# Kernel tuning notes

Measured on AMD Instinct MI355X. Metric: run time of the kernel, lower is better.

## Reference

```python
import jax, jax.numpy as jnp
import numpy as np

N_USER = 100000
N_ITEM = 100000
SUPP = 10000
B = 1024
L = 50
S = 256
H = 4
E = 64
HID = 64


def setup_inputs() -> dict:
    key = jax.random.key(0)
    ks = jax.random.split(key, 32)
    f32 = jnp.float32
    inp = {}
    # forward int args
    inp["x"] = jax.random.randint(ks[0], (B, 2), 0, N_USER)
    inp["src_his"] = jax.random.randint(ks[1], (B, L), 0, N_ITEM)
    inp["src_hl"] = jax.random.randint(ks[2], (B,), 0, L)
    inp["tgt_his"] = jax.random.randint(ks[3], (B, L), 0, N_ITEM)
    inp["tgt_hl"] = jax.random.randint(ks[4], (B,), 0, L)
    # precomputed neighbor sampling: [2 get_user_emb calls, H heads, B, S]
    inp["sample_idx"] = jax.random.randint(ks[5], (2, H, B, S), 0, SUPP)
    inp["supp_users"] = jax.random.randint(ks[6], (SUPP,), 0, N_USER)
    # embedding tables (xavier-ish small scale)
    inp["src_user_emb"] = jax.random.normal(ks[7], (N_USER, E), f32) * 0.1
    inp["src_item_emb"] = jax.random.normal(ks[8], (N_ITEM, E), f32) * 0.1
    inp["tgt_user_emb"] = jax.random.normal(ks[9], (N_USER, E), f32) * 0.1
    inp["tgt_item_emb"] = jax.random.normal(ks[10], (N_ITEM, E), f32) * 0.1
    # attention / aggregation weights, stored [in, out]
    s = 1.0 / np.sqrt(E)
    inp["W_att_w"] = jax.random.normal(ks[11], (E, E), f32) * s
    inp["W_att_b"] = jnp.full((E,), 0.1, f32)
    inp["W_agg_w"] = jax.random.normal(ks[12], (E, E), f32) * s
    # per-head GAT projections, batched over heads
    inp["Wq"] = jax.random.normal(ks[13], (H, E, E), f32) * s
    inp["Wk"] = jax.random.normal(ks[14], (H, E, E), f32) * s
    inp["Wv"] = jax.random.normal(ks[15], (H, E, E), f32) * s
    inp["W_out"] = jax.random.normal(ks[16], (H * E, E), f32) * (1.0 / np.sqrt(H * E))
    # scoring MLP
    inp["l1_w"] = jax.random.normal(ks[17], (2 * E, HID), f32) * (1.0 / np.sqrt(2 * E))
    inp["l1_b"] = jnp.full((HID,), 0.1, f32)
    inp["l2_w"] = jax.random.normal(ks[18], (HID, E), f32) * (1.0 / np.sqrt(HID))
    inp["l2_b"] = jnp.full((E,), 0.1, f32)
    inp["l3_w"] = jax.random.normal(ks[19], (E, 1), f32) * s
    inp["l3_b"] = jnp.full((1,), 0.1, f32)
    return inp


def reference(x, src_his, src_hl, tgt_his, tgt_hl, sample_idx, supp_users,
              src_user_emb, src_item_emb, tgt_user_emb, tgt_item_emb,
              W_att_w, W_att_b, W_agg_w, Wq, Wk, Wv, W_out,
              l1_w, l1_b, l2_w, l2_b, l3_w, l3_b):
    user_id = x[:, 0]
    item_id = x[:, 1]

    def user_fea_encode(his, hl, user_table):
        # NOTE: original always gathers from src_model.item_embedding (even for tgt)
        Lh = his.shape[1]
        valid = jnp.arange(Lh)[None, :] < hl[:, None]          # [B,L]
        hist = src_item_emb[his] * valid[..., None]             # [B,L,E], padded rows zeroed
        u = user_table[user_id]                                 # [B,E]
        keyt = jnp.tanh(hist @ W_att_w + W_att_b)               # [B,L,E]
        pad = hist.sum(-1) == 0                                 # [B,L]
        att = jnp.einsum('ble,be->bl', keyt, u)
        # faithful masked_softmax: masked scores set to 0 BEFORE exp (exp(0)=1 still contributes)
        att = jnp.where(pad, 0.0, att)
        e = jnp.exp(att)
        att = e / (jnp.sum(e, axis=1, keepdims=True) + 1e-12)
        out = jnp.einsum('bl,ble->be', att, hist)
        return out @ W_agg_w                                    # W_agg has no bias

    def get_user_emb(fea, idx):
        # idx: [H,B,S] indices into supp_users; all heads batched in one einsum chain
        neigh = tgt_user_emb[supp_users[idx]]                   # [H,B,S,E]
        q = jnp.einsum('be,heo->hbo', fea, Wq)                  # [H,B,O]
        k = jnp.einsum('hbse,heo->hbso', neigh, Wk)             # [H,B,S,O]
        attn = jax.nn.softmax(jnp.einsum('hbo,hbso->hbs', q, k), axis=-1)
        ctx = jnp.einsum('hbs,hbso->hbo', attn, k)              # weighted sum over neighbors
        g = jnp.einsum('hbo,hop->hbp', ctx, Wv)                 # [H,B,O]
        g = jnp.transpose(g, (1, 0, 2)).reshape(fea.shape[0], -1)  # concat heads -> [B,H*O]
        return g @ W_out

    user_src_fea = user_fea_encode(src_his, src_hl, src_user_emb)
    user_emb = get_user_emb(user_src_fea, sample_idx[0])
    item_emb = tgt_item_emb[item_id]
    user_tgt_fea = user_fea_encode(tgt_his, tgt_hl, tgt_user_emb)
    hybrid_tgt_emb = get_user_emb(user_tgt_fea, sample_idx[1])

    x_t = jnp.concatenate([hybrid_tgt_emb, item_emb], axis=1)
    x1_t = jnp.tanh(x_t @ l1_w + l1_b)
    x2_t = jnp.tanh(x1_t @ l2_w + l2_b)
    x3_t = (x2_t @ l3_w + l3_b).reshape(-1)

    output = jnp.sum(user_emb * item_emb, axis=1)
    out_emb_s = user_emb * item_emb
    # (output, output_t, out_emb_s, out_emb_t); train=False branch (sim/domain heads are None)
    return (output, x3_t, out_emb_s, x2_t)
```

## Files before the change

### kernel.cpp

```cpp
#include <hip/hip_runtime.h>

constexpr int B    = 1024;
constexpr int L    = 50;
constexpr int S    = 256;
constexpr int H    = 4;
constexpr int E    = 64;
constexpr int HID  = 64;
constexpr int SUPP = 10000;

__device__ __forceinline__ float lanebc(float v, int l) {
    return __int_as_float(__builtin_amdgcn_readlane(__float_as_int(v), l));
}

__device__ __forceinline__ float bcdot64(float v, const float* w) {
    float a0 = 0.0f, a1 = 0.0f;
#pragma unroll
    for (int i = 0; i < E; i += 2) {
        a0 += lanebc(v, i)     * w[i];
        a1 += lanebc(v, i + 1) * w[i + 1];
    }
    return a0 + a1;
}

__global__ __launch_bounds__(256) void pre_kernel(
    const int* __restrict__ x,
    const int* __restrict__ src_his,
    const int* __restrict__ src_hl,
    const int* __restrict__ tgt_his,
    const int* __restrict__ tgt_hl,
    const float* __restrict__ item_emb,
    const float* __restrict__ src_user_emb,
    const float* __restrict__ tgt_user_emb,
    const int* __restrict__ supp_users,
    const float* __restrict__ W_att_w,
    const float* __restrict__ W_att_b,
    const float* __restrict__ W_agg_w,
    const float* __restrict__ Wq,
    const float* __restrict__ Wk,
    float* __restrict__ qout,
    float* __restrict__ K_supp)
{
    const int tid  = threadIdx.x;
    const int lane = tid & 63;
    const int wave = tid >> 6;

    if (blockIdx.y == 2) {
        const int h = wave;
        float wcol[E];
#pragma unroll
        for (int i = 0; i < E; i++) wcol[i] = Wk[h * E * E + i * E + lane];

        const int base = blockIdx.x * 4;
#pragma unroll
        for (int m = 0; m < 3; m++) {
            const int j0 = base + m * 4096;
            if (j0 >= SUPP) break;
            const int u0 = supp_users[j0];
            const int u1 = supp_users[j0 + 1];
            const int u2 = supp_users[j0 + 2];
            const int u3 = supp_users[j0 + 3];
            const float e0 = tgt_user_emb[(size_t)u0 * E + lane];
            const float e1 = tgt_user_emb[(size_t)u1 * E + lane];
            const float e2 = tgt_user_emb[(size_t)u2 * E + lane];
            const float e3 = tgt_user_emb[(size_t)u3 * E + lane];
            float a0 = 0.0f, a1 = 0.0f, a2 = 0.0f, a3 = 0.0f;
#pragma unroll
            for (int i = 0; i < E; i++) {
                a0 += lanebc(e0, i) * wcol[i];
                a1 += lanebc(e1, i) * wcol[i];
                a2 += lanebc(e2, i) * wcol[i];
                a3 += lanebc(e3, i) * wcol[i];
            }
            float* dst = K_supp + ((size_t)h * SUPP + j0) * E + lane;
            dst[0]     = a0;
            dst[E]     = a1;
            dst[2 * E] = a2;
            dst[3 * E] = a3;
        }
        return;
    }

    __shared__ float sHist[L * E];
    __shared__ float sAtt[L];
    __shared__ float sPart[4][E];
    __shared__ float sOut[E];

    const int b    = blockIdx.x;
    const int call = blockIdx.y;

    const int* his = call ? tgt_his : src_his;
    const int* hl  = call ? tgt_hl  : src_hl;
    const float* user_table = call ? tgt_user_emb : src_user_emb;

    float wcol[E];
#pragma unroll
    for (int i = 0; i < E; i++) wcol[i] = W_att_w[i * E + lane];

    const int uid    = x[2 * b];
    const float uv   = user_table[(size_t)uid * E + lane];
    const float bias = W_att_b[lane];
    const int hlen   = hl[b];

#pragma unroll
    for (int i = 0; i < 13; i++) {
        const int l = wave + 4 * i;
        if (l < L) {
            const int it = his[b * L + l];
            sHist[l * E + lane] = (l < hlen) ? item_emb[(size_t)it * E + lane] : 0.0f;
        }
    }
    __syncthreads();

#pragma unroll
    for (int g = 0; g < 3; g++) {
        const int l0 = wave + 16 * g;
        const int l1 = l0 + 4, l2 = l0 + 8, l3 = l0 + 12;
        const float h0 = sHist[l0 * E + lane];
        const float h1 = sHist[l1 * E + lane];
        const float h2 = sHist[l2 * E + lane];
        const float h3 = sHist[l3 * E + lane];
        float a0 = bias, a1 = bias, a2 = bias, a3 = bias;
#pragma unroll
        for (int i = 0; i < E; i++) {
            a0 += lanebc(h0, i) * wcol[i];
            a1 += lanebc(h1, i) * wcol[i];
            a2 += lanebc(h2, i) * wcol[i];
            a3 += lanebc(h3, i) * wcol[i];
        }
        float p0 = tanhf(a0) * uv, p1 = tanhf(a1) * uv;
        float p2 = tanhf(a2) * uv, p3 = tanhf(a3) * uv;
        float s0 = h0, s1 = h1, s2 = h2, s3 = h3;
#pragma unroll
        for (int off = 32; off; off >>= 1) {
            p0 += __shfl_xor(p0, off); s0 += __shfl_xor(s0, off);
            p1 += __shfl_xor(p1, off); s1 += __shfl_xor(s1, off);
            p2 += __shfl_xor(p2, off); s2 += __shfl_xor(s2, off);
            p3 += __shfl_xor(p3, off); s3 += __shfl_xor(s3, off);
        }
        if (lane == 0) {
            sAtt[l0] = (s0 == 0.0f) ? 0.0f : p0;
            sAtt[l1] = (s1 == 0.0f) ? 0.0f : p1;
            sAtt[l2] = (s2 == 0.0f) ? 0.0f : p2;
            sAtt[l3] = (s3 == 0.0f) ? 0.0f : p3;
        }
    }
    {
        const int l = wave + 48;
        if (l < L) {
            const float hv = sHist[l * E + lane];
            const float a = bias + bcdot64(hv, wcol);
            float part = tanhf(a) * uv;
            float hsum = hv;
#pragma unroll
            for (int off = 32; off; off >>= 1) {
                part += __shfl_xor(part, off);
                hsum += __shfl_xor(hsum, off);
            }
            if (lane == 0) sAtt[l] = (hsum == 0.0f) ? 0.0f : part;
        }
    }
    __syncthreads();

    if (wave == 0) {
        float v = (lane < L) ? expf(sAtt[lane]) : 0.0f;
        float s = v;
#pragma unroll
        for (int off = 32; off; off >>= 1) s += __shfl_xor(s, off);
        const float denom = s + 1e-12f;
        if (lane < L) sAtt[lane] = v / denom;
    }
    __syncthreads();

    {
        float c0 = 0.0f, c1 = 0.0f;
        for (int l = wave; l < L; l += 8) c0 += sAtt[l] * sHist[l * E + lane];
        for (int l = wave + 4; l < L; l += 8) c1 += sAtt[l] * sHist[l * E + lane];
        sPart[wave][lane] = c0 + c1;
    }
    __syncthreads();
    if (tid < E) sOut[tid] = sPart[0][tid] + sPart[1][tid] + sPart[2][tid] + sPart[3][tid];
    __syncthreads();

    {
        float g0 = 0.0f, g1 = 0.0f;
#pragma unroll
        for (int k = 0; k < 16; k += 2) {
            const int i = wave * 16 + k;
            g0 += sOut[i]     * W_agg_w[i * E + lane];
            g1 += sOut[i + 1] * W_agg_w[(i + 1) * E + lane];
        }
        sPart[wave][lane] = g0 + g1;
    }
    __syncthreads();

    const float fval = sPart[0][lane] + sPart[1][lane] + sPart[2][lane] + sPart[3][lane];
    const float* Wqh = Wq + wave * E * E;
    float q0 = 0.0f, q1 = 0.0f;
#pragma unroll
    for (int i = 0; i < E; i += 2) {
        q0 += lanebc(fval, i)     * Wqh[i * E + lane];
        q1 += lanebc(fval, i + 1) * Wqh[(i + 1) * E + lane];
    }
    qout[(((call * H) + wave) * B + b) * E + lane] = q0 + q1;
}

__global__ __launch_bounds__(256) void attn_kernel(
    const int* __restrict__ sample_idx,
    const float* __restrict__ K_supp,
    const float* __restrict__ qarr,
    const float* __restrict__ Wv,
    float* __restrict__ gout)
{
    __shared__ float sRed[8];
    __shared__ float sCtx[4][E];
    __shared__ float sC[E];
    __shared__ float sG[4][E];

    const int bid  = blockIdx.x;
    const int h    = bid & 3;
    const int call = (bid >> 2) & 1;
    const int b    = bid >> 3;
    const int tid  = threadIdx.x;
    const int lane = tid & 63;
    const int wave = tid >> 6;
    const int u    = lane & 15;
    const int rsub = lane >> 4;
    const int s0   = wave * 64;

    const int* idx = sample_idx + (((call * H) + h) * B + b) * S;
    const float* Kh = K_supp + (size_t)h * SUPP * E;
    const float4 qu = *(const float4*)(qarr + ((size_t)(((call * H) + h) * B + b)) * E + 4 * u);

    float4 kreg[16];
    float mylogit = 0.0f;
#pragma unroll
    for (int i = 0; i < 16; i++) {
        const int j = idx[s0 + 4 * i + rsub];
        kreg[i] = *(const float4*)(Kh + (size_t)j * E + 4 * u);
        float part = kreg[i].x * qu.x + kreg[i].y * qu.y
                   + kreg[i].z * qu.z + kreg[i].w * qu.w;
#pragma unroll
        for (int off = 1; off < 16; off <<= 1) part += __shfl_xor(part, off);
        mylogit = (u == i) ? part : mylogit;
    }

    float m = mylogit;
#pragma unroll
    for (int off = 32; off; off >>= 1) m = fmaxf(m, __shfl_xor(m, off));
    if (lane == 0) sRed[wave] = m;
    __syncthreads();
    const float mx = fmaxf(fmaxf(sRed[0], sRed[1]), fmaxf(sRed[2], sRed[3]));
    const float ex = expf(mylogit - mx);
    float sm = ex;
#pragma unroll
    for (int off = 32; off; off >>= 1) sm += __shfl_xor(sm, off);
    if (lane == 0) sRed[4 + wave] = sm;
    __syncthreads();
    const float denom = sRed[4] + sRed[5] + sRed[6] + sRed[7];
    const float pval = ex / denom;

    float4 cacc = make_float4(0.0f, 0.0f, 0.0f, 0.0f);
#pragma unroll
    for (int i = 0; i < 16; i++) {
        const float p = __shfl(pval, (lane & 48) + i);
        cacc.x += p * kreg[i].x;
        cacc.y += p * kreg[i].y;
        cacc.z += p * kreg[i].z;
        cacc.w += p * kreg[i].w;
    }
#pragma unroll
    for (int off = 16; off <= 32; off <<= 1) {
        cacc.x += __shfl_xor(cacc.x, off);
        cacc.y += __shfl_xor(cacc.y, off);
        cacc.z += __shfl_xor(cacc.z, off);
        cacc.w += __shfl_xor(cacc.w, off);
    }
    if (lane < 16) *(float4*)(&sCtx[wave][u * 4]) = cacc;
    __syncthreads();
    if (wave == 0) {
        sC[lane] = sCtx[0][lane] + sCtx[1][lane] + sCtx[2][lane] + sCtx[3][lane];
    }
    __syncthreads();

    const float* Wvh = Wv + h * E * E;
    float g0 = 0.0f, g1 = 0.0f;
#pragma unroll
    for (int k = 0; k < 16; k += 2) {
        const int c = wave * 16 + k;
        g0 += sC[c]     * Wvh[c * E + lane];
        g1 += sC[c + 1] * Wvh[(c + 1) * E + lane];
    }
    sG[wave][lane] = g0 + g1;
    __syncthreads();
    if (wave == 0) {
        gout[((size_t)(call * B) + b) * (H * E) + h * E + lane] =
            sG[0][lane] + sG[1][lane] + sG[2][lane] + sG[3][lane];
    }
}

__global__ __launch_bounds__(256) void final_kernel(
    const int* __restrict__ x,
    const float* __restrict__ tgt_item_emb,
    const float* __restrict__ gsrc,
    const float* __restrict__ gtgt,
    const float* __restrict__ W_out,
    const float* __restrict__ l1_w,
    const float* __restrict__ l1_b,
    const float* __restrict__ l2_w,
    const float* __restrict__ l2_b,
    const float* __restrict__ l3_w,
    const float* __restrict__ l3_b,
    float* __restrict__ out)
{
    __shared__ float sPart[4][E];
    __shared__ float sHyb[E];
    __shared__ float sItem[E];
    __shared__ float sX1[HID];

    const int b    = blockIdx.x;
    const int tid  = threadIdx.x;
    const int lane = tid & 63;
    const int wave = tid >> 6;

    if (tid < E) {
        const int item = x[2 * b + 1];
        sItem[tid] = tgt_item_emb[(size_t)item * E + tid];
    }

    const float* grow = (wave < 2) ? (gsrc + (size_t)b * (H * E))
                                   : (gtgt + (size_t)b * (H * E));
    const int i0 = (wave & 1) * 128;
    float a0 = 0.0f, a1 = 0.0f, a2 = 0.0f, a3 = 0.0f;
    for (int i = i0; i < i0 + 128; i += 4) {
        a0 += grow[i]     * W_out[i * E + lane];
        a1 += grow[i + 1] * W_out[(i + 1) * E + lane];
        a2 += grow[i + 2] * W_out[(i + 2) * E + lane];
        a3 += grow[i + 3] * W_out[(i + 3) * E + lane];
    }
    sPart[wave][lane] = (a0 + a1) + (a2 + a3);
    __syncthreads();

    if (wave == 0) {
        const float ue = sPart[0][lane] + sPart[1][lane];
        const float prod = ue * sItem[lane];
        out[2 * B + b * E + lane] = prod;
        float s = prod;
#pragma unroll
        for (int off = 32; off; off >>= 1) s += __shfl_xor(s, off);
        if (lane == 0) out[b] = s;
    }
    if (wave == 1) {
        sHyb[lane] = sPart[2][lane] + sPart[3][lane];
    }
    __syncthreads();

    {
        float b0 = 0.0f, b1 = 0.0f, b2 = 0.0f, b3 = 0.0f;
#pragma unroll
        for (int k = 0; k < 32; k += 4) {
            const int i = wave * 32 + k;
            const float v0 = (i < 64)     ? sHyb[i]          : sItem[i - 64];
            const float v1 = (i + 1 < 64) ? sHyb[i + 1]      : sItem[i + 1 - 64];
            const float v2 = (i + 2 < 64) ? sHyb[i + 2]      : sItem[i + 2 - 64];
            const float v3 = (i + 3 < 64) ? sHyb[i + 3]      : sItem[i + 3 - 64];
            b0 += v0 * l1_w[i * HID + lane];
            b1 += v1 * l1_w[(i + 1) * HID + lane];
            b2 += v2 * l1_w[(i + 2) * HID + lane];
            b3 += v3 * l1_w[(i + 3) * HID + lane];
        }
        sPart[wave][lane] = (b0 + b1) + (b2 + b3);
    }
    __syncthreads();

    if (wave == 0) {
        const float a = l1_b[lane] + sPart[0][lane] + sPart[1][lane]
                      + sPart[2][lane] + sPart[3][lane];
        sX1[lane] = tanhf(a);
    }
    __syncthreads();

    {
        float c0 = 0.0f, c1 = 0.0f, c2 = 0.0f, c3 = 0.0f;
#pragma unroll
        for (int k = 0; k < 16; k += 4) {
            const int i = wave * 16 + k;
            c0 += sX1[i]     * l2_w[i * E + lane];
            c1 += sX1[i + 1] * l2_w[(i + 1) * E + lane];
            c2 += sX1[i + 2] * l2_w[(i + 2) * E + lane];
            c3 += sX1[i + 3] * l2_w[(i + 3) * E + lane];
        }
        sPart[wave][lane] = (c0 + c1) + (c2 + c3);
    }
    __syncthreads();

    if (wave == 0) {
        const float a = l2_b[lane] + sPart[0][lane] + sPart[1][lane]
                      + sPart[2][lane] + sPart[3][lane];
        const float x2 = tanhf(a);
        out[2 * B + B * E + b * E + lane] = x2;
        float p = x2 * l3_w[lane];
#pragma unroll
        for (int off = 32; off; off >>= 1) p += __shfl_xor(p, off);
        if (lane == 0) out[B + b] = p + l3_b[0];
    }
}

extern "C" void kernel_launch(void* const* d_in, const int* in_sizes, int n_in,
                              void* d_out, int out_size, void* d_ws, size_t ws_size,
                              hipStream_t stream) {
    const int*   x            = (const int*)d_in[0];
    const int*   src_his      = (const int*)d_in[1];
    const int*   src_hl       = (const int*)d_in[2];
    const int*   tgt_his      = (const int*)d_in[3];
    const int*   tgt_hl       = (const int*)d_in[4];
    const int*   sample_idx   = (const int*)d_in[5];
    const int*   supp_users   = (const int*)d_in[6];
    const float* src_user_emb = (const float*)d_in[7];
    const float* src_item_emb = (const float*)d_in[8];
    const float* tgt_user_emb = (const float*)d_in[9];
    const float* tgt_item_emb = (const float*)d_in[10];
    const float* W_att_w      = (const float*)d_in[11];
    const float* W_att_b      = (const float*)d_in[12];
    const float* W_agg_w      = (const float*)d_in[13];
    const float* Wq           = (const float*)d_in[14];
    const float* Wk           = (const float*)d_in[15];
    const float* Wv           = (const float*)d_in[16];
    const float* W_out        = (const float*)d_in[17];
    const float* l1_w         = (const float*)d_in[18];
    const float* l1_b         = (const float*)d_in[19];
    const float* l2_w         = (const float*)d_in[20];
    const float* l2_b         = (const float*)d_in[21];
    const float* l3_w         = (const float*)d_in[22];
    const float* l3_b         = (const float*)d_in[23];

    float* ws      = (float*)d_ws;
    float* qarr    = ws;
    float* K_supp  = qarr + 2 * H * B * E;
    float* garr    = K_supp + H * SUPP * E;
    float* out     = (float*)d_out;

    pre_kernel<<<dim3(B, 3), 256, 0, stream>>>(
        x, src_his, src_hl, tgt_his, tgt_hl, src_item_emb,
        src_user_emb, tgt_user_emb, supp_users,
        W_att_w, W_att_b, W_agg_w, Wq, Wk, qarr, K_supp);
    attn_kernel<<<dim3(B * H * 2), 256, 0, stream>>>(
        sample_idx, K_supp, qarr, Wv, garr);
    final_kernel<<<dim3(B), 256, 0, stream>>>(
        x, tgt_item_emb, garr, garr + B * H * E, W_out,
        l1_w, l1_b, l2_w, l2_b, l3_w, l3_b, out);
}
```

Measured before the change: 297.9 us.

## Fold Wq·Wkᵀ and Wk·Wv into combined matrices to gather raw support embeddings

After: 281.2 us. 1.06x faster.

```diff
diff --git a/kernel.cpp b/kernel.cpp
--- a/kernel.cpp
+++ b/kernel.cpp
@@ -37,45 +37,51 @@
     const float* __restrict__ W_agg_w,
     const float* __restrict__ Wq,
     const float* __restrict__ Wk,
-    float* __restrict__ qout,
-    float* __restrict__ K_supp)
+    const float* __restrict__ Wv,
+    float* __restrict__ feaout,
+    float* __restrict__ E_supp,
+    float* __restrict__ Mmat,
+    float* __restrict__ WkWv)
 {
     const int tid  = threadIdx.x;
     const int lane = tid & 63;
     const int wave = tid >> 6;
 
     if (blockIdx.y == 2) {
-        const int h = wave;
-        float wcol[E];
-#pragma unroll
-        for (int i = 0; i < E; i++) wcol[i] = Wk[h * E * E + i * E + lane];
-
-        const int base = blockIdx.x * 4;
-#pragma unroll
-        for (int m = 0; m < 3; m++) {
-            const int j0 = base + m * 4096;
-            if (j0 >= SUPP) break;
-            const int u0 = supp_users[j0];
-            const int u1 = supp_users[j0 + 1];
-            const int u2 = supp_users[j0 + 2];
-            const int u3 = supp_users[j0 + 3];
-            const float e0 = tgt_user_emb[(size_t)u0 * E + lane];
-            const float e1 = tgt_user_emb[(size_t)u1 * E + lane];
-            const float e2 = tgt_user_emb[(size_t)u2 * E + lane];
-            const float e3 = tgt_user_emb[(size_t)u3 * E + lane];
-            float a0 = 0.0f, a1 = 0.0f, a2 = 0.0f, a3 = 0.0f;
-#pragma unroll
-            for (int i = 0; i < E; i++) {
-                a0 += lanebc(e0, i) * wcol[i];
-                a1 += lanebc(e1, i) * wcol[i];
-                a2 += lanebc(e2, i) * wcol[i];
-                a3 += lanebc(e3, i) * wcol[i];
+        const int bid = blockIdx.x;
+        if (bid < H) {
+            const int h = bid;
+            float wrow[E];
+#pragma unroll
+            for (int o = 0; o < E; o++) wrow[o] = Wk[h * E * E + lane * E + o];
+#pragma unroll
+            for (int k = 0; k < 16; k++) {
+                const int i = wave * 16 + k;
+                float a0 = 0.0f, a1 = 0.0f;
+#pragma unroll
+                for (int o = 0; o < E; o += 2) {
+                    a0 += Wq[h * E * E + i * E + o]     * wrow[o];
+                    a1 += Wq[h * E * E + i * E + o + 1] * wrow[o + 1];
+                }
+                Mmat[h * E * E + i * E + lane] = a0 + a1;
             }
-            float* dst = K_supp + ((size_t)h * SUPP + j0) * E + lane;
-            dst[0]     = a0;
-            dst[E]     = a1;
-            dst[2 * E] = a2;
-            dst[3 * E] = a3;
+#pragma unroll
+            for (int o = 0; o < E; o++) wrow[o] = Wv[h * E * E + o * E + lane];
+#pragma unroll
+            for (int k = 0; k < 16; k++) {
+                const int i = wave * 16 + k;
+                float a0 = 0.0f, a1 = 0.0f;
+#pragma unroll
+                for (int o = 0; o < E; o += 2) {
+                    a0 += Wk[h * E * E + i * E + o]     * wrow[o];
+                    a1 += Wk[h * E * E + i * E + o + 1] * wrow[o + 1];
+                }
+                WkWv[h * E * E + i * E + lane] = a0 + a1;
+            }
+        }
+        for (int j = bid + (wave << 10); j < SUPP; j += 4096) {
+            E_supp[(size_t)j * E + lane] =
+                tgt_user_emb[(size_t)supp_users[j] * E + lane];
         }
         return;
     }
@@ -193,24 +199,21 @@
     }
     __syncthreads();
 
-    const float fval = sPart[0][lane] + sPart[1][lane] + sPart[2][lane] + sPart[3][lane];
-    const float* Wqh = Wq + wave * E * E;
-    float q0 = 0.0f, q1 = 0.0f;
-#pragma unroll
-    for (int i = 0; i < E; i += 2) {
-        q0 += lanebc(fval, i)     * Wqh[i * E + lane];
-        q1 += lanebc(fval, i + 1) * Wqh[(i + 1) * E + lane];
-    }
-    qout[(((call * H) + wave) * B + b) * E + lane] = q0 + q1;
+    if (wave == 0) {
+        feaout[((size_t)call * B + b) * E + lane] =
+            sPart[0][lane] + sPart[1][lane] + sPart[2][lane] + sPart[3][lane];
+    }
 }
 
 __global__ __launch_bounds__(256) void attn_kernel(
     const int* __restrict__ sample_idx,
-    const float* __restrict__ K_supp,
-    const float* __restrict__ qarr,
-    const float* __restrict__ Wv,
+    const float* __restrict__ E_supp,
+    const float* __restrict__ fea,
+    const float* __restrict__ Mmat,
+    const float* __restrict__ WkWv,
     float* __restrict__ gout)
 {
+    __shared__ float sQ[E];
     __shared__ float sRed[8];
     __shared__ float sCtx[4][E];
     __shared__ float sC[E];
@@ -227,16 +230,28 @@
     const int rsub = lane >> 4;
     const int s0   = wave * 64;
 
+    if (wave == 0) {
+        const float feav = fea[((size_t)call * B + b) * E + lane];
+        const float* Mh = Mmat + h * E * E;
+        float a0 = 0.0f, a1 = 0.0f;
+#pragma unroll
+        for (int i = 0; i < E; i += 2) {
+            a0 += lanebc(feav, i)     * Mh[i * E + lane];
+            a1 += lanebc(feav, i + 1) * Mh[(i + 1) * E + lane];
+        }
+        sQ[lane] = a0 + a1;
+    }
+    __syncthreads();
+
     const int* idx = sample_idx + (((call * H) + h) * B + b) * S;
-    const float* Kh = K_supp + (size_t)h * SUPP * E;
-    const float4 qu = *(const float4*)(qarr + ((size_t)(((call * H) + h) * B + b)) * E + 4 * u);
+    const float4 qu = *(const float4*)(sQ + 4 * u);
 
     float4 kreg[16];
     float mylogit = 0.0f;
 #pragma unroll
     for (int i = 0; i < 16; i++) {
         const int j = idx[s0 + 4 * i + rsub];
-        kreg[i] = *(const float4*)(Kh + (size_t)j * E + 4 * u);
+        kreg[i] = *(const float4*)(E_supp + (size_t)j * E + 4 * u);
         float part = kreg[i].x * qu.x + kreg[i].y * qu.y
                    + kreg[i].z * qu.z + kreg[i].w * qu.w;
 #pragma unroll
@@ -282,13 +297,13 @@
     }
     __syncthreads();
 
-    const float* Wvh = Wv + h * E * E;
+    const float* Wh = WkWv + h * E * E;
     float g0 = 0.0f, g1 = 0.0f;
 #pragma unroll
     for (int k = 0; k < 16; k += 2) {
         const int c = wave * 16 + k;
-        g0 += sC[c]     * Wvh[c * E + lane];
-        g1 += sC[c + 1] * Wvh[(c + 1) * E + lane];
+        g0 += sC[c]     * Wh[c * E + lane];
+        g1 += sC[c + 1] * Wh[(c + 1) * E + lane];
     }
     sG[wave][lane] = g0 + g1;
     __syncthreads();
@@ -359,10 +374,10 @@
 #pragma unroll
         for (int k = 0; k < 32; k += 4) {
             const int i = wave * 32 + k;
-            const float v0 = (i < 64)     ? sHyb[i]          : sItem[i - 64];
-            const float v1 = (i + 1 < 64) ? sHyb[i + 1]      : sItem[i + 1 - 64];
-            const float v2 = (i + 2 < 64) ? sHyb[i + 2]      : sItem[i + 2 - 64];
-            const float v3 = (i + 3 < 64) ? sHyb[i + 3]      : sItem[i + 3 - 64];
+            const float v0 = (i < 64)     ? sHyb[i]     : sItem[i - 64];
+            const float v1 = (i + 1 < 64) ? sHyb[i + 1] : sItem[i + 1 - 64];
+            const float v2 = (i + 2 < 64) ? sHyb[i + 2] : sItem[i + 2 - 64];
+            const float v3 = (i + 3 < 64) ? sHyb[i + 3] : sItem[i + 3 - 64];
             b0 += v0 * l1_w[i * HID + lane];
             b1 += v1 * l1_w[(i + 1) * HID + lane];
             b2 += v2 * l1_w[(i + 2) * HID + lane];
@@ -434,17 +449,20 @@
     const float* l3_b         = (const float*)d_in[23];
 
     float* ws      = (float*)d_ws;
-    float* qarr    = ws;
-    float* K_supp  = qarr + 2 * H * B * E;
-    float* garr    = K_supp + H * SUPP * E;
+    float* fea     = ws;
+    float* E_supp  = fea + 2 * B * E;
+    float* Mmat    = E_supp + SUPP * E;
+    float* WkWv    = Mmat + H * E * E;
+    float* garr    = WkWv + H * E * E;
     float* out     = (float*)d_out;
 
     pre_kernel<<<dim3(B, 3), 256, 0, stream>>>(
         x, src_his, src_hl, tgt_his, tgt_hl, src_item_emb,
         src_user_emb, tgt_user_emb, supp_users,
-        W_att_w, W_att_b, W_agg_w, Wq, Wk, qarr, K_supp);
+        W_att_w, W_att_b, W_agg_w, Wq, Wk, Wv,
+        fea, E_supp, Mmat, WkWv);
     attn_kernel<<<dim3(B * H * 2), 256, 0, stream>>>(
-        sample_idx, K_supp, qarr, Wv, garr);
+        sample_idx, E_supp, fea, Mmat, WkWv, garr);
     final_kernel<<<dim3(B), 256, 0, stream>>>(
         x, tgt_item_emb, garr, garr + B * H * E, W_out,
         l1_w, l1_b, l2_w, l2_b, l3_w, l3_b, out);
```
